# Optimization experiments

Measured on AMD Instinct MI355X. Metric: run time of the kernel, lower is better.

The kernel has to match this reference:

```python
import jax, jax.numpy as jnp
import numpy as np

B, S, H, DH, D, FD, FU = 4, 256, 12, 64, 768, 2048, 2048


def setup_inputs() -> dict:
    key = jax.random.key(0)
    ks = jax.random.split(key, 12)
    s = 0.02  # typical init scale for weights
    return {
        "resid_pre": jax.random.normal(ks[0], (B, S, D), jnp.float32),
        "ln_scale": jax.random.uniform(ks[1], (B, S, 1), jnp.float32, 0.5, 2.0),
        "probs": jax.nn.softmax(jax.random.normal(ks[2], (B, H, S, S), jnp.float32), axis=-1),
        "W_O": jax.random.normal(ks[3], (H, DH, D), jnp.float32) * s,
        "W_V": jax.random.normal(ks[4], (H, D, DH), jnp.float32) * s,
        "enc_W": jax.random.normal(ks[5], (FD, D), jnp.float32) * s,
        "enc_b": jax.random.normal(ks[6], (FD,), jnp.float32) * s,
        "b_dec": jax.random.normal(ks[7], (D,), jnp.float32) * s,
        "up_dec_W": jax.random.normal(ks[8], (D, FU), jnp.float32) * s,
        "up_b_dec": jax.random.normal(ks[9], (D,), jnp.float32) * s,
        "pruned_features": jax.random.normal(ks[10], (B, S, FU), jnp.float32),
        "connection_mask": jax.random.randint(ks[11], (FD, FU), 0, 2, jnp.int32),
    }


def reference(resid_pre, ln_scale, probs, W_O, W_V, enc_W, enc_b, b_dec,
              up_dec_W, up_b_dec, pruned_features, connection_mask):
    # W_OV: [h, d_model(in), d_model(out)]
    W_OV = jnp.einsum('hko,hmk->hmo', W_O, W_V)
    mask = connection_mask.astype(resid_pre.dtype)

    # --- initial contributions ---
    act_ln = resid_pre / ln_scale                                  # [b,s,d]
    pre_moving = jnp.einsum('bsi,hio,fo->bshf', act_ln, W_OV, enc_W)  # [b,s,h,f_down]
    approx = jnp.einsum('bhqk,bkhf->bqf', probs, pre_moving)       # [b,q,f_down]

    # --- pruned contributions (one upstream AE) ---
    virtual = jnp.einsum('fo,hio,iu->hfu', enc_W, W_OV, up_dec_W) * mask[None]
    up_ln = pruned_features / ln_scale                             # [b,k,f_up]
    post_ov = jnp.einsum('bku,hfu->bhkf', up_ln, virtual)          # [b,h,k,f_down]
    approx = approx + jnp.einsum('bhqk,bhkf->bqf', probs, post_ov)

    # --- bias terms ---
    approx = approx + enc_b[None, None] - (enc_W @ b_dec)[None, None]
    ub_ln = up_b_dec[None, None] / ln_scale                        # [b,s,d]
    ub_post = jnp.einsum('hmd,bsm->bsd', W_OV, ub_ln)              # attn path through OV
    approx = approx + jnp.einsum('fd,bsd->bsf', enc_W, ub_post)
    return approx
```

## Files before the change

### kernel.cpp

```cpp
#include <hip/hip_runtime.h>
#include <hip/hip_bf16.h>
#include <stdint.h>

typedef __bf16 bf16;
typedef __bf16 bf16x8 __attribute__((ext_vector_type(8)));
typedef __bf16 bf16x4 __attribute__((ext_vector_type(4)));
typedef float f32x4 __attribute__((ext_vector_type(4)));

#define AS1 __attribute__((address_space(1)))
#define AS3 __attribute__((address_space(3)))


__device__ __forceinline__ void gld16(const bf16* g, bf16* l) {
  __builtin_amdgcn_global_load_lds((AS1 void*)g, (AS3 void*)l, 16, 0, 0);
}

__global__ void k_sentinel(float* __restrict__ out) {
  int i = blockIdx.x * 256 + threadIdx.x;
  if (i < 2097152) out[i] = 1048576.0f;
}

__global__ void k_prep(const float* __restrict__ lns, float* __restrict__ invln,
                       const float* __restrict__ enc_W, bf16* __restrict__ encWb,
                       const float* __restrict__ probs, bf16* __restrict__ probsT,
                       const int* __restrict__ cmask, bf16* __restrict__ maskb,
                       const float* __restrict__ W_O, bf16* __restrict__ WOb,
                       const float* __restrict__ resid, bf16* __restrict__ Xb,
                       bf16* __restrict__ BgTail, long ldTail) {
  const int bid = blockIdx.x, t = threadIdx.x;
  if (bid < 1) {
    for (int k = 0; k < 4; k++) { int j = t + k * 256; invln[j] = 1.0f / lns[j]; }
  } else if (bid < 1537) {
    long idx = ((long)(bid - 1) * 256 + t) * 4;
    float4 v = *(const float4*)(enc_W + idx);
    bf16x4 o; o[0]=(bf16)v.x; o[1]=(bf16)v.y; o[2]=(bf16)v.z; o[3]=(bf16)v.w;
    *(bf16x4*)(encWb + idx) = o;
  } else if (bid < 4609) {
    long idx = ((long)(bid - 1537) * 256 + t) * 4;
    int s = (int)(idx & 255), q = (int)((idx >> 8) & 255);
    int hb = (int)(idx >> 16), h = hb % 12, b = hb / 12;
    float4 v = *(const float4*)(probs + idx);
    bf16x4 o; o[0]=(bf16)v.x; o[1]=(bf16)v.y; o[2]=(bf16)v.z; o[3]=(bf16)v.w;
    *(bf16x4*)(probsT + (long)b * 786432 + (long)q * 3072 + h * 256 + s) = o;
  } else if (bid < 8705) {
    long idx = ((long)(bid - 4609) * 256 + t) * 4;
    int4 v = *(const int4*)(cmask + idx);
    bf16x4 o; o[0]=(bf16)(float)v.x; o[1]=(bf16)(float)v.y;
    o[2]=(bf16)(float)v.z; o[3]=(bf16)(float)v.w;
    *(bf16x4*)(maskb + idx) = o;
  } else if (bid < 9857) {
    long idx = ((long)(bid - 8705) * 256 + t) * 4;
    int o = (int)(idx % 768), r = (int)((idx / 768) & 127), h = (int)(idx / (768 * 128));
    bf16x4 ov;
    if (r < 64) {
      float4 v = *(const float4*)(W_O + (long)(h * 64 + r) * 768 + o);
      ov[0]=(bf16)v.x; ov[1]=(bf16)v.y; ov[2]=(bf16)v.z; ov[3]=(bf16)v.w;
    } else { ov[0]=ov[1]=ov[2]=ov[3]=(bf16)0.0f; }
    *(bf16x4*)(WOb + idx) = ov;
  } else if (bid < 10625) {
    long idx = ((long)(bid - 9857) * 256 + t) * 4;
    float il = 1.0f / lns[idx / 768];
    float4 v = *(const float4*)(resid + idx);
    bf16x4 o; o[0]=(bf16)(v.x*il); o[1]=(bf16)(v.y*il);
    o[2]=(bf16)(v.z*il); o[3]=(bf16)(v.w*il);
    *(bf16x4*)(Xb + idx) = o;
  } else {
    long idx = ((long)(bid - 10625) * 256 + t) * 4;
    int f = (int)(idx / 768), d = (int)(idx % 768);
    float4 v = *(const float4*)(enc_W + idx);
    bf16x4 o; o[0]=(bf16)v.x; o[1]=(bf16)v.y; o[2]=(bf16)v.z; o[3]=(bf16)v.w;
    *(bf16x4*)(BgTail + (long)f * ldTail + d) = o;
  }
}

__global__ void k_prepT(const float* __restrict__ wv, bf16* __restrict__ WVt,
                        const float* __restrict__ wo, bf16* __restrict__ W_Ot,
                        const float* __restrict__ updW, bf16* __restrict__ updWt,
                        const float* __restrict__ pr, const float* __restrict__ lns,
                        bf16* __restrict__ Ut) {
  __shared__ float tile[32][33];
  const int bid = blockIdx.x;
  int lane = threadIdx.x & 31, rg = threadIdx.x >> 5;
  if (bid < 1152) {
    int r0 = bid;
    int x = r0 % 4, y = (r0 / 4) % 24, h = r0 / 96;
    int k0 = x * 32, i0 = y * 32;
    if (k0 < 64) {
      for (int r = rg; r < 32; r += 8)
        tile[r][lane] = wv[((long)(h * 768 + i0 + r)) * 64 + k0 + lane];
      __syncthreads();
      for (int r = rg; r < 32; r += 8)
        WVt[((long)h * 128 + k0 + r) * 768 + i0 + lane] = (bf16)tile[lane][r];
    } else {
      for (int r = rg; r < 32; r += 8)
        WVt[((long)h * 128 + k0 + r) * 768 + i0 + lane] = (bf16)0.0f;
    }
  } else if (bid < 1728) {
    int r0 = bid - 1152;
    int x = r0 % 2, y = (r0 / 2) % 24, h = r0 / 48;
    int k0 = x * 32, o0 = y * 32;
    for (int r = rg; r < 32; r += 8)
      tile[r][lane] = wo[((long)(h * 64 + k0 + r)) * 768 + o0 + lane];
    __syncthreads();
    for (int r = rg; r < 32; r += 8)
      W_Ot[((long)(h * 768 + o0 + r)) * 64 + k0 + lane] = (bf16)tile[lane][r];
  } else if (bid < 3264) {
    int r0 = bid - 1728;
    int u0 = (r0 % 64) * 32, i0 = (r0 / 64) * 32;
    for (int r = rg; r < 32; r += 8)
      tile[r][lane] = updW[((long)(i0 + r)) * 2048 + u0 + lane];
    __syncthreads();
    for (int r = rg; r < 32; r += 8)
      updWt[((long)(u0 + r)) * 768 + i0 + lane] = (bf16)tile[lane][r];
  } else {
    int r0 = bid - 3264;
    int u0 = (r0 % 64) * 32, s0 = ((r0 / 64) % 8) * 32, b = r0 / 512;
    for (int r = rg; r < 32; r += 8) {
      int s = s0 + r;
      tile[r][lane] = pr[((long)(b * 256 + s)) * 2048 + u0 + lane] *
                      (1.0f / lns[b * 256 + s]);
    }
    __syncthreads();
    for (int r = rg; r < 32; r += 8)
      Ut[((long)b * 2048 + u0 + r) * 256 + s0 + lane] = (bf16)tile[lane][r];
  }
}

__global__ void k_sred(const float* __restrict__ Sp, bf16* __restrict__ dst, long ldd) {
  int i = blockIdx.x * 256 + threadIdx.x;
  if (i < 196608) {
    long idx = (long)i * 4;
    int m = (int)(idx / 768), o = (int)(idx % 768);
    float4 v = *(const float4*)(Sp + idx);
    float4 a = *(const float4*)(Sp + 786432 + idx);
    float4 b = *(const float4*)(Sp + 2 * 786432 + idx);
    float4 c = *(const float4*)(Sp + 3 * 786432 + idx);
    v.x += a.x + b.x + c.x; v.y += a.y + b.y + c.y;
    v.z += a.z + b.z + c.z; v.w += a.w + b.w + c.w;
    bf16x4 ov;
    ov[0] = (bf16)v.x; ov[1] = (bf16)v.y; ov[2] = (bf16)v.z; ov[3] = (bf16)v.w;
    *(bf16x4*)(dst + (long)m * ldd + o) = ov;
  }
}


__device__ __forceinline__ float blk_reduce(float s) {
  __shared__ float red[256];
  red[threadIdx.x] = s; __syncthreads();
  for (int o = 128; o > 0; o >>= 1) {
    if ((int)threadIdx.x < o) red[threadIdx.x] += red[threadIdx.x + o];
    __syncthreads();
  }
  float r = red[0]; __syncthreads();
  return r;
}

__global__ void k_bias_t(const float* __restrict__ W_V, const float* __restrict__ up_b,
                         float* __restrict__ t_hk) {
  int j = blockIdx.x, h = j >> 6, k = j & 63;
  float s = 0.f;
  for (int m = threadIdx.x; m < 768; m += 256)
    s += W_V[((long)(h * 768 + m)) * 64 + k] * up_b[m];
  float r = blk_reduce(s);
  if (threadIdx.x == 0) t_hk[j] = r;
}

__global__ void k_bias_w(const float* __restrict__ W_O, const float* __restrict__ t_hk,
                         float* __restrict__ w) {
  int d = blockIdx.x;
  float s = 0.f;
  for (int j = threadIdx.x; j < 768; j += 256)
    s += W_O[(long)j * 768 + d] * t_hk[j];
  float r = blk_reduce(s);
  if (threadIdx.x == 0) w[d] = r;
}

__global__ void k_bias_c(const float* __restrict__ enc_W, const float* __restrict__ enc_b,
                         const float* __restrict__ b_dec, const float* __restrict__ w,
                         float* __restrict__ c0, float* __restrict__ c1) {
  int f = blockIdx.x;
  float s0 = 0.f, s1 = 0.f;
  for (int d = threadIdx.x; d < 768; d += 256) {
    float e = enc_W[(long)f * 768 + d];
    s0 += e * b_dec[d];
    s1 += e * w[d];
  }
  float r0 = blk_reduce(s0);
  float r1 = blk_reduce(s1);
  if (threadIdx.x == 0) { c0[f] = enc_b[f] - r0; c1[f] = r1; }
}

__global__ __launch_bounds__(256)
void gemm_bt(const bf16* __restrict__ A, const bf16* __restrict__ B, void* __restrict__ Cv,
             int M, int N, int K,
             long lda, long ldb, long ldc,
             int batchH,
             long sa_b, long sa_h, long sb_b, long sb_h, long sc_b, long sc_h,
             int mode, int kChunk,
             const bf16* __restrict__ mask, long mask_ld)
{
  __shared__ __align__(16) bf16 SMEM[16384];
  bf16* Asm = SMEM;
  bf16* Bsm = SMEM + 8192;

  const int t = threadIdx.x;

  const int nbx = gridDim.x, nby = gridDim.y;
  const int nxy = nbx * nby;
  int orig = blockIdx.x + nbx * blockIdx.y;
  int qq = nxy >> 3, rr = nxy & 7;
  int xcd = orig & 7, lid = orig >> 3;
  int swz = (xcd < rr) ? (xcd * (qq + 1) + lid)
                       : (rr * (qq + 1) + (xcd - rr) * qq + lid);
  const int m0 = (swz % nby) * 128;
  const int n0 = (swz / nby) * 128;

  long aoff, boff, coff;
  int k0, k1;
  if (mode == 4) {
    int z = blockIdx.z;
    int bb = z / batchH, kc = z - bb * batchH;
    aoff = (long)bb * sa_b;
    boff = (long)bb * sb_b;
    coff = (long)bb * sc_b + (long)kc * sc_h;
    k0 = kc * kChunk; k1 = k0 + kChunk; if (k1 > K) k1 = K;
  } else if (mode >= 2) {
    int z = blockIdx.z;
    aoff = 0; boff = 0;
    coff = (long)z * (long)M * ldc;
    k0 = z * kChunk; k1 = k0 + kChunk; if (k1 > K) k1 = K;
  } else {
    int z = blockIdx.z;
    int bb = z / batchH, hh = z - bb * batchH;
    aoff = (long)bb * sa_b + (long)hh * sa_h;
    boff = (long)bb * sb_b + (long)hh * sb_h;
    coff = (long)bb * sc_b + (long)hh * sc_h;
    k0 = 0; k1 = K;
  }

  const bf16* Ab = A + aoff + (long)m0 * lda;
  const bf16* Bb = B + boff + (long)n0 * ldb;

  const int r0 = t >> 3;
  const int g8 = t & 7;

  const int L = t & 63, w = t >> 6;
  const int wm = (w & 1) * 64, wn = (w >> 1) * 64;
  const int r16 = L & 15, q = L >> 4;

  f32x4 acc[4][4];
#pragma unroll
  for (int i = 0; i < 4; i++)
#pragma unroll
    for (int j = 0; j < 4; j++) acc[i][j] = (f32x4){0.f, 0.f, 0.f, 0.f};

  for (int kt = k0; kt < k1; kt += 64) {
#pragma unroll
    for (int j = 0; j < 4; j++) {
      int row = j * 32 + r0;
      int sc = ((g8 ^ (row & 7)) << 3);
      gld16(Ab + (long)row * lda + (kt + sc), &Asm[j * 2048 + t * 8]);
      gld16(Bb + (long)row * ldb + (kt + sc), &Bsm[j * 2048 + t * 8]);
    }
    __syncthreads();

#pragma unroll
    for (int h2 = 0; h2 < 2; h2++) {
      bf16x8 af[4], bfr[4];
#pragma unroll
      for (int i = 0; i < 4; i++) {
        int ra = wm + i * 16 + r16;
        af[i]  = *(const bf16x8*)&Asm[ra * 64 + ((((h2 << 2) + q) ^ (ra & 7)) << 3)];
        int rb = wn + i * 16 + r16;
        bfr[i] = *(const bf16x8*)&Bsm[rb * 64 + ((((h2 << 2) + q) ^ (rb & 7)) << 3)];
      }
#pragma unroll
      for (int mi = 0; mi < 4; mi++)
#pragma unroll
        for (int ni = 0; ni < 4; ni++)
          acc[mi][ni] = __builtin_amdgcn_mfma_f32_16x16x32_bf16(af[mi], bfr[ni], acc[mi][ni], 0, 0, 0);
    }
    __syncthreads();
  }

  if (mode >= 2) {
    float* C = (float*)Cv;
#pragma unroll
    for (int mi = 0; mi < 4; mi++)
#pragma unroll
      for (int ni = 0; ni < 4; ni++)
#pragma unroll
        for (int r = 0; r < 4; r++) {
          int gm = m0 + wm + mi * 16 + q * 4 + r;
          int gn = n0 + wn + ni * 16 + r16;
          long idx = coff + (long)gm * ldc + gn;
          float v = acc[mi][ni][r];
          if (mode == 3) v += C[idx];
          C[idx] = v;
        }
  } else {
    bf16* C = (bf16*)Cv;
    bf16* lbuf = SMEM;
    const int lrbase = (wm >> 6) * 32 + q * 4;
    const int lr_r = t >> 2;
    const int colg = (t & 3) * 32;
#pragma unroll
    for (int hh = 0; hh < 2; hh++) {
#pragma unroll
      for (int m2 = 0; m2 < 2; m2++) {
        int mi = hh * 2 + m2;
#pragma unroll
        for (int ni = 0; ni < 4; ni++) {
          int col = wn + ni * 16 + r16;
#pragma unroll
          for (int r = 0; r < 4; r++)
            lbuf[(lrbase + m2 * 16 + r) * 136 + col] = (bf16)acc[mi][ni][r];
        }
      }
      __syncthreads();
      int gm = m0 + (lr_r >> 5) * 64 + hh * 32 + (lr_r & 31);
#pragma unroll
      for (int s = 0; s < 4; s++) {
        bf16x8 v = *(const bf16x8*)&lbuf[lr_r * 136 + colg + 8 * s];
        int gn = n0 + colg + 8 * s;
        if (mode == 1) {
          bf16x8 mv = *(const bf16x8*)&mask[(long)gm * mask_ld + gn];
#pragma unroll
          for (int j = 0; j < 8; j++) v[j] = (bf16)((float)v[j] * (float)mv[j]);
        }
        *(bf16x8*)&C[coff + (long)gm * ldc + gn] = v;
      }
      __syncthreads();
    }
  }
}

__global__ __launch_bounds__(512, 2)
void gemm_fp2(const bf16* __restrict__ A, const bf16* __restrict__ B,
              float* __restrict__ C,
              int M, int N, int K, long lda, long ldb, long ldc,
              int mode, int kChunk)
{
  __shared__ __align__(16) bf16 SM[2][2][16384];

  const int t = threadIdx.x;

  const int nz = gridDim.z;
  int fid = blockIdx.x + gridDim.x * (blockIdx.y + gridDim.y * blockIdx.z);
  const int z  = fid % nz;
  const int t2 = fid / nz;
  const int m0 = (t2 >> 3) * 256;
  const int n0 = (t2 & 7) * 256;

  const long coff = (long)z * (long)M * ldc;
  int k0 = z * kChunk, k1 = k0 + kChunk; if (k1 > K) k1 = K;
  const int NT = (k1 > k0) ? (k1 - k0) >> 6 : 0;

  const bf16* Ab = A + (long)m0 * lda + k0;
  const bf16* Bb = B + (long)n0 * ldb + k0;

  const int sr = t >> 3;
  const int g8 = t & 7;

  const int L = t & 63, w = t >> 6;
  const int wm = (w & 1) * 128;
  const int wn = (w >> 1) * 64;
  const int r16 = L & 15, q = L >> 4;

  f32x4 acc[8][4];
#pragma unroll
  for (int i = 0; i < 8; i++)
#pragma unroll
    for (int j = 0; j < 4; j++) acc[i][j] = (f32x4){0.f, 0.f, 0.f, 0.f};

  auto stage = [&](int tt, int buf) {
    const bf16* Ap = Ab + (long)tt * 64;
    const bf16* Bp = Bb + (long)tt * 64;
#pragma unroll
    for (int j = 0; j < 4; j++) {
      int row = j * 64 + sr;
      int sc = ((g8 ^ (row & 7)) << 3);
      gld16(Ap + (long)row * lda + sc, &SM[buf][0][j * 4096 + t * 8]);
    }
#pragma unroll
    for (int j = 0; j < 4; j++) {
      int row = j * 64 + sr;
      int sc = ((g8 ^ (row & 7)) << 3);
      gld16(Bp + (long)row * ldb + sc, &SM[buf][1][j * 4096 + t * 8]);
    }
  };

  if (NT >= 1) stage(0, 0);

  for (int tt = 0; tt < NT; tt++) {
    if (tt + 1 < NT) {
      stage(tt + 1, (tt + 1) & 1);
      asm volatile("s_waitcnt vmcnt(8)" ::: "memory");
    } else {
      asm volatile("s_waitcnt vmcnt(0)" ::: "memory");
    }
    __builtin_amdgcn_s_barrier();

    const bf16* As = &SM[tt & 1][0][0];
    const bf16* Bs = &SM[tt & 1][1][0];
#pragma unroll
    for (int h2 = 0; h2 < 2; h2++) {
      bf16x8 af[8], bfr[4];
#pragma unroll
      for (int i = 0; i < 8; i++) {
        int ra = wm + i * 16 + r16;
        af[i]  = *(const bf16x8*)&As[ra * 64 + ((((h2 << 2) + q) ^ (ra & 7)) << 3)];
      }
#pragma unroll
      for (int i = 0; i < 4; i++) {
        int rb = wn + i * 16 + r16;
        bfr[i] = *(const bf16x8*)&Bs[rb * 64 + ((((h2 << 2) + q) ^ (rb & 7)) << 3)];
      }
#pragma unroll
      for (int mi = 0; mi < 8; mi++)
#pragma unroll
        for (int ni = 0; ni < 4; ni++)
          acc[mi][ni] = __builtin_amdgcn_mfma_f32_16x16x32_bf16(af[mi], bfr[ni], acc[mi][ni], 0, 0, 0);
    }
    __builtin_amdgcn_s_barrier();
  }

#pragma unroll
  for (int mi = 0; mi < 8; mi++)
#pragma unroll
    for (int ni = 0; ni < 4; ni++)
#pragma unroll
      for (int r = 0; r < 4; r++) {
        int gm = m0 + wm + mi * 16 + q * 4 + r;
        int gn = n0 + wn + ni * 16 + r16;
        long idx = coff + (long)gm * ldc + gn;
        float v = acc[mi][ni][r];
        if (mode == 3) v += C[idx];
        C[idx] = v;
      }
}

__global__ void k_out(const float* __restrict__ Cp, const float* __restrict__ c0,
                      const float* __restrict__ c1, const float* __restrict__ invln,
                      float* __restrict__ out, int nsplit) {
  int i4 = blockIdx.x * 256 + threadIdx.x;
  long i = (long)i4 * 4;
  int n = (int)(i & 2047), m = (int)(i >> 11);
  float4 v = *(const float4*)(Cp + i);
  for (int z = 1; z < nsplit; z++) {
    float4 u = *(const float4*)(Cp + i + (long)z * 2097152);
    v.x += u.x; v.y += u.y; v.z += u.z; v.w += u.w;
  }
  float il = invln[m];
  float4 a = *(const float4*)(c0 + n);
  float4 b = *(const float4*)(c1 + n);
  v.x += a.x + b.x * il;
  v.y += a.y + b.y * il;
  v.z += a.z + b.z * il;
  v.w += a.w + b.w * il;
  *(float4*)(out + i) = v;
}


extern "C" void kernel_launch(void* const* d_in, const int* in_sizes, int n_in,
                              void* d_out, int out_size, void* d_ws, size_t ws_size,
                              hipStream_t stream) {
  (void)out_size;
  float* out = (float*)d_out;

  int iresid = -1, iln = -1, iprobs = -1, iencb = -1, ipruned = -1, imask = -1;
  int iwo = -1, iwv = -1, iencw = -1, iupdw = -1, ibdec = -1, iupb = -1;
  for (int i = 0; i < n_in; i++) {
    switch (in_sizes[i]) {
      case 786432:  iresid  = i; break;
      case 1024:    iln     = i; break;
      case 3145728: iprobs  = i; break;
      case 2048:    iencb   = i; break;
      case 2097152: ipruned = i; break;
      case 4194304: imask   = i; break;
      case 589824:  if (iwo   < 0) iwo   = i; else iwv   = i; break;
      case 1572864: if (iencw < 0) iencw = i; else iupdw = i; break;
      case 768:     if (ibdec < 0) ibdec = i; else iupb  = i; break;
      default: break;
    }
  }
  bool ok = n_in == 12 && iresid >= 0 && iln >= 0 && iprobs >= 0 && iencb >= 0 &&
            ipruned >= 0 && imask >= 0 && iwo >= 0 && iwv >= 0 && iencw >= 0 &&
            iupdw >= 0 && ibdec >= 0 && iupb >= 0;
  if (!ok) { k_sentinel<<<8192, 256, 0, stream>>>(out); return; }

  const float* resid = (const float*)d_in[iresid];
  const float* lns   = (const float*)d_in[iln];
  const float* probs = (const float*)d_in[iprobs];
  const float* W_O   = (const float*)d_in[iwo];
  const float* W_V   = (const float*)d_in[iwv];
  const float* enc_W = (const float*)d_in[iencw];
  const float* enc_b = (const float*)d_in[iencb];
  const float* b_dec = (const float*)d_in[ibdec];
  const float* updW  = (const float*)d_in[iupdw];
  const float* up_b  = (const float*)d_in[iupb];
  const float* pruned= (const float*)d_in[ipruned];
  const int*   cmask = (const int*)d_in[imask];

  auto pad = [](size_t b) -> size_t { return (b + 255) & ~(size_t)255; };
  const size_t prepB = pad(2359296) + pad(2359296) + pad(3145728) + pad(1572864) +
                       pad(3145728) + pad(1179648) + pad(3145728) + pad(18874368) +
                       pad(12582912);
  const size_t persB = pad(6291456) + pad(4194304) + pad(6291456) + pad(6291456) +
                       pad(8388608) + pad(4096) + pad(3072) + pad(3072) +
                       pad(8192) + pad(8192);
  auto needB = [&](int g, int ns) -> size_t {
    size_t cp = (size_t)ns * 8388608;
    size_t ov = prepB > cp ? prepB : cp;
    long KA = (long)g * 2048 + 768;
    size_t ab = pad((size_t)1024 * KA * 2) + pad((size_t)2048 * KA * 2);
    return ov + persB + ab + (2ull << 20);
  };
  const int cgs[14] = {12, 12, 12, 6, 6, 4, 3, 2, 2, 1, 1, 1, 1, 1};
  const int cns[14] = { 8,  4, 2, 8, 4, 4, 4, 4, 2, 8, 4, 2, 2, 1};
  int gs = 0, nsplit = 0;
  for (int ci = 0; ci < 14; ci++) {
    if (needB(cgs[ci], cns[ci]) <= ws_size) { gs = cgs[ci]; nsplit = cns[ci]; break; }
  }
  if (gs == 0) { gs = 1; nsplit = 1; }

  const long KA = (long)gs * 2048 + 768;

  char* p = (char*)d_ws;
  auto alloc = [&](size_t bytes) -> char* {
    char* r = p; p += (bytes + 255) & ~(size_t)255; return r;
  };
  char* overlayBase = p;
  bf16*  WOb    = (bf16*)alloc(12ull * 128 * 768 * 2);
  bf16*  WVt    = (bf16*)alloc(12ull * 128 * 768 * 2);
  bf16*  updWt  = (bf16*)alloc(2048ull * 768 * 2);
  bf16*  Xb     = (bf16*)alloc(1024ull * 768 * 2);
  bf16*  encWb  = (bf16*)alloc(2048ull * 768 * 2);
  bf16*  W_Ot   = (bf16*)alloc(12ull * 768 * 64 * 2);
  bf16*  T1     = (bf16*)alloc(12ull * 1024 * 128 * 2);
  bf16*  T3     = (bf16*)alloc(4ull * 768 * 3072 * 2);
  float* Sp     = (float*)alloc(4ull * 1024 * 768 * 4);
  {
    size_t used = (size_t)(p - overlayBase);
    size_t cp = (size_t)nsplit * 8388608;
    p = overlayBase + (used > cp ? used : cp);
  }
  float* Cpart  = (float*)overlayBase;
  bf16*  G_t    = (bf16*)alloc(12ull * 2048 * 128 * 2);
  bf16*  Ut     = (bf16*)alloc(4ull * 2048 * 256 * 2);
  bf16*  E1     = (bf16*)alloc(12ull * 2048 * 128 * 2);
  bf16*  probsT = (bf16*)alloc(4ull * 256 * 3072 * 2);
  bf16*  maskb  = (bf16*)alloc(2048ull * 2048 * 2);
  float* invln  = (float*)alloc(1024 * 4);
  float* t_hk   = (float*)alloc(768 * 4);
  float* wv     = (float*)alloc(768 * 4);
  float* c0     = (float*)alloc(2048 * 4);
  float* c1     = (float*)alloc(2048 * 4);
  bf16*  A_g    = (bf16*)alloc((size_t)1024 * KA * 2);
  bf16*  B_g    = (bf16*)alloc((size_t)2048 * KA * 2);

  k_prep<<<12161, 256, 0, stream>>>(lns, invln, enc_W, encWb, probs, probsT,
                                    cmask, maskb, W_O, WOb, resid, Xb,
                                    B_g + (long)gs * 2048, KA);
  k_prepT<<<5312, 256, 0, stream>>>(W_V, WVt, W_O, W_Ot, updW, updWt,
                                    pruned, lns, Ut);
  k_bias_t<<<768, 256, 0, stream>>>(W_V, up_b, t_hk);
  k_bias_w<<<768, 256, 0, stream>>>(W_O, t_hk, wv);
  k_bias_c<<<2048, 256, 0, stream>>>(enc_W, enc_b, b_dec, wv, c0, c1);

  gemm_bt<<<dim3(1, 16, 24), 256, 0, stream>>>(
      encWb, WOb, E1, 2048, 128, 768,
      768, 768, 128, 12,
      (long)(updWt - encWb), 0,
      (long)(WVt - WOb), (long)128 * 768,
      (long)(G_t - E1), (long)2048 * 128,
      0, 0, nullptr, 0);

  gemm_bt<<<dim3(1, 8, 12), 256, 0, stream>>>(
      Xb, WVt, T1, 1024, 128, 768,
      768, 768, 128, 12,
      0, 0, 0, (long)128 * 768, 0, (long)1024 * 128,
      0, 0, nullptr, 0);

  gemm_bt<<<dim3(2, 6, 48), 256, 0, stream>>>(
      W_Ot, T1, T3, 768, 256, 64,
      64, 128, 3072, 12,
      0, (long)768 * 64, (long)256 * 128, (long)1024 * 128, 2359296, 256,
      0, 0, nullptr, 0);

  gemm_bt<<<dim3(6, 2, 16), 256, 0, stream>>>(
      probsT, T3, Sp, 256, 768, 3072,
      3072, 3072, 768, 4,
      786432, 0, 2359296, 0, 196608, 786432,
      4, 768, nullptr, 0);

  k_sred<<<768, 256, 0, stream>>>(Sp, A_g + (long)gs * 2048, KA);

  for (int g = 0; g < 12 / gs; g++) {
    gemm_bt<<<dim3(16, 16, gs), 256, 0, stream>>>(
        E1 + (long)g * gs * 2048 * 128, G_t + (long)g * gs * 2048 * 128, B_g,
        2048, 2048, 64,
        128, 128, KA, gs,
        0, (long)2048 * 128, 0, (long)2048 * 128, 0, 2048,
        1, 0, maskb, 2048);

    gemm_bt<<<dim3(16, 2, 4 * gs), 256, 0, stream>>>(
        probsT + (long)g * gs * 256, Ut, A_g,
        256, 2048, 256,
        3072, 256, KA, gs,
        786432, 256, (long)2048 * 256, 0, 256 * KA, 2048,
        0, 0, nullptr, 0);

    int Kthis = (g == 0) ? (int)KA : gs * 2048;
    int kc = ((Kthis / nsplit + 63) / 64) * 64;
    gemm_fp2<<<dim3(8, 4, nsplit), 512, 0, stream>>>(
        A_g, B_g, Cpart,
        1024, 2048, Kthis,
        KA, KA, 2048,
        (g == 0) ? 2 : 3, kc);
  }

  k_out<<<2048, 256, 0, stream>>>(Cpart, c0, c1, invln, out, nsplit);
}
```

Measured before the change: 406.7 us.

## Fuse bias, reduction and batched GEMM launches into fewer kernels

The three bias kernels are folded into extra blocks of the prep, transpose and split-reduce kernels. The E1/G_t GEMM and the X·W_V GEMM become one batched launch: buffers are laid out contiguously and the third batch clamps its B operand and exits early beyond its smaller M. The per-group loop is replaced by a single pass over all heads. The goal is to cut launch count and serial tail gaps, at the cost of assuming the full group size fits in memory.

```diff
diff --git a/kernel.cpp b/kernel.cpp
--- a/kernel.cpp
+++ b/kernel.cpp
@@ -26,7 +26,10 @@
                        const int* __restrict__ cmask, bf16* __restrict__ maskb,
                        const float* __restrict__ W_O, bf16* __restrict__ WOb,
                        const float* __restrict__ resid, bf16* __restrict__ Xb,
-                       bf16* __restrict__ BgTail, long ldTail) {
+                       bf16* __restrict__ BgTail, long ldTail,
+                       const float* __restrict__ W_V, const float* __restrict__ up_b,
+                       float* __restrict__ t_hk) {
+  __shared__ float red[256];
   const int bid = blockIdx.x, t = threadIdx.x;
   if (bid < 1) {
     for (int k = 0; k < 4; k++) { int j = t + k * 256; invln[j] = 1.0f / lns[j]; }
@@ -64,12 +67,21 @@
     bf16x4 o; o[0]=(bf16)(v.x*il); o[1]=(bf16)(v.y*il);
     o[2]=(bf16)(v.z*il); o[3]=(bf16)(v.w*il);
     *(bf16x4*)(Xb + idx) = o;
-  } else {
+  } else if (bid < 12161) {
     long idx = ((long)(bid - 10625) * 256 + t) * 4;
     int f = (int)(idx / 768), d = (int)(idx % 768);
     float4 v = *(const float4*)(enc_W + idx);
     bf16x4 o; o[0]=(bf16)v.x; o[1]=(bf16)v.y; o[2]=(bf16)v.z; o[3]=(bf16)v.w;
     *(bf16x4*)(BgTail + (long)f * ldTail + d) = o;
+  } else {
+    int h = bid - 12161;
+    int k = t & 63, qd = t >> 6;
+    float s = 0.f;
+    for (int m = qd; m < 768; m += 4)
+      s += W_V[((long)(h * 768 + m)) * 64 + k] * up_b[m];
+    red[t] = s; __syncthreads();
+    if (qd == 0)
+      t_hk[h * 64 + k] = red[k] + red[64 + k] + red[128 + k] + red[192 + k];
   }
 }
 
@@ -77,7 +89,8 @@
                         const float* __restrict__ wo, bf16* __restrict__ W_Ot,
                         const float* __restrict__ updW, bf16* __restrict__ updWt,
                         const float* __restrict__ pr, const float* __restrict__ lns,
-                        bf16* __restrict__ Ut) {
+                        bf16* __restrict__ Ut,
+                        const float* __restrict__ t_hk, float* __restrict__ wvec) {
   __shared__ float tile[32][33];
   const int bid = blockIdx.x;
   int lane = threadIdx.x & 31, rg = threadIdx.x >> 5;
@@ -112,7 +125,7 @@
     __syncthreads();
     for (int r = rg; r < 32; r += 8)
       updWt[((long)(u0 + r)) * 768 + i0 + lane] = (bf16)tile[lane][r];
-  } else {
+  } else if (bid < 5312) {
     int r0 = bid - 3264;
     int u0 = (r0 % 64) * 32, s0 = ((r0 / 64) % 8) * 32, b = r0 / 512;
     for (int r = rg; r < 32; r += 8) {
@@ -123,12 +136,29 @@
     __syncthreads();
     for (int r = rg; r < 32; r += 8)
       Ut[((long)b * 2048 + u0 + r) * 256 + s0 + lane] = (bf16)tile[lane][r];
-  }
-}
-
-__global__ void k_sred(const float* __restrict__ Sp, bf16* __restrict__ dst, long ldd) {
-  int i = blockIdx.x * 256 + threadIdx.x;
-  if (i < 196608) {
+  } else {
+    int d = bid - 5312;
+    float* red = &tile[0][0];
+    float s = 0.f;
+    for (int j = threadIdx.x; j < 768; j += 256)
+      s += wo[(long)j * 768 + d] * t_hk[j];
+    red[threadIdx.x] = s; __syncthreads();
+    for (int o = 128; o > 0; o >>= 1) {
+      if ((int)threadIdx.x < o) red[threadIdx.x] += red[threadIdx.x + o];
+      __syncthreads();
+    }
+    if (threadIdx.x == 0) wvec[d] = red[0];
+  }
+}
+
+__global__ void k_misc(const float* __restrict__ Sp, bf16* __restrict__ dst, long ldd,
+                       const float* __restrict__ enc_W, const float* __restrict__ enc_b,
+                       const float* __restrict__ b_dec, const float* __restrict__ w,
+                       float* __restrict__ c0, float* __restrict__ c1) {
+  __shared__ float red[512];
+  const int bid = blockIdx.x, t = threadIdx.x;
+  if (bid < 768) {
+    int i = bid * 256 + t;
     long idx = (long)i * 4;
     int m = (int)(idx / 768), o = (int)(idx % 768);
     float4 v = *(const float4*)(Sp + idx);
@@ -140,54 +170,21 @@
     bf16x4 ov;
     ov[0] = (bf16)v.x; ov[1] = (bf16)v.y; ov[2] = (bf16)v.z; ov[3] = (bf16)v.w;
     *(bf16x4*)(dst + (long)m * ldd + o) = ov;
-  }
-}
-
-
-__device__ __forceinline__ float blk_reduce(float s) {
-  __shared__ float red[256];
-  red[threadIdx.x] = s; __syncthreads();
-  for (int o = 128; o > 0; o >>= 1) {
-    if ((int)threadIdx.x < o) red[threadIdx.x] += red[threadIdx.x + o];
-    __syncthreads();
-  }
-  float r = red[0]; __syncthreads();
-  return r;
-}
-
-__global__ void k_bias_t(const float* __restrict__ W_V, const float* __restrict__ up_b,
-                         float* __restrict__ t_hk) {
-  int j = blockIdx.x, h = j >> 6, k = j & 63;
-  float s = 0.f;
-  for (int m = threadIdx.x; m < 768; m += 256)
-    s += W_V[((long)(h * 768 + m)) * 64 + k] * up_b[m];
-  float r = blk_reduce(s);
-  if (threadIdx.x == 0) t_hk[j] = r;
-}
-
-__global__ void k_bias_w(const float* __restrict__ W_O, const float* __restrict__ t_hk,
-                         float* __restrict__ w) {
-  int d = blockIdx.x;
-  float s = 0.f;
-  for (int j = threadIdx.x; j < 768; j += 256)
-    s += W_O[(long)j * 768 + d] * t_hk[j];
-  float r = blk_reduce(s);
-  if (threadIdx.x == 0) w[d] = r;
-}
-
-__global__ void k_bias_c(const float* __restrict__ enc_W, const float* __restrict__ enc_b,
-                         const float* __restrict__ b_dec, const float* __restrict__ w,
-                         float* __restrict__ c0, float* __restrict__ c1) {
-  int f = blockIdx.x;
-  float s0 = 0.f, s1 = 0.f;
-  for (int d = threadIdx.x; d < 768; d += 256) {
-    float e = enc_W[(long)f * 768 + d];
-    s0 += e * b_dec[d];
-    s1 += e * w[d];
-  }
-  float r0 = blk_reduce(s0);
-  float r1 = blk_reduce(s1);
-  if (threadIdx.x == 0) { c0[f] = enc_b[f] - r0; c1[f] = r1; }
+  } else {
+    int f = bid - 768;
+    float s0 = 0.f, s1 = 0.f;
+    for (int d = t; d < 768; d += 256) {
+      float e = enc_W[(long)f * 768 + d];
+      s0 += e * b_dec[d];
+      s1 += e * w[d];
+    }
+    red[t] = s0; red[256 + t] = s1; __syncthreads();
+    for (int o = 128; o > 0; o >>= 1) {
+      if (t < o) { red[t] += red[t + o]; red[256 + t] += red[256 + t + o]; }
+      __syncthreads();
+    }
+    if (t == 0) { c0[f] = enc_b[f] - red[0]; c1[f] = red[256]; }
+  }
 }
 
 __global__ __launch_bounds__(256)
@@ -197,7 +194,8 @@
              int batchH,
              long sa_b, long sa_h, long sb_b, long sb_h, long sc_b, long sc_h,
              int mode, int kChunk,
-             const bf16* __restrict__ mask, long mask_ld)
+             const bf16* __restrict__ mask, long mask_ld,
+             int bbBmax, int bbM2)
 {
   __shared__ __align__(16) bf16 SMEM[16384];
   bf16* Asm = SMEM;
@@ -232,8 +230,10 @@
   } else {
     int z = blockIdx.z;
     int bb = z / batchH, hh = z - bb * batchH;
+    if (bbM2 && bb >= 2 && m0 >= bbM2) return;
+    int bbB = bb < bbBmax ? bb : bbBmax;
     aoff = (long)bb * sa_b + (long)hh * sa_h;
-    boff = (long)bb * sb_b + (long)hh * sb_h;
+    boff = (long)bbB * sb_b + (long)hh * sb_h;
     coff = (long)bb * sc_b + (long)hh * sc_h;
     k0 = 0; k1 = K;
   }
@@ -502,18 +502,23 @@
   const float* pruned= (const float*)d_in[ipruned];
   const int*   cmask = (const int*)d_in[imask];
 
-  auto pad = [](size_t b) -> size_t { return (b + 255) & ~(size_t)255; };
-  const size_t prepB = pad(2359296) + pad(2359296) + pad(3145728) + pad(1572864) +
-                       pad(3145728) + pad(1179648) + pad(3145728) + pad(18874368) +
-                       pad(12582912);
-  const size_t persB = pad(6291456) + pad(4194304) + pad(6291456) + pad(6291456) +
-                       pad(8388608) + pad(4096) + pad(3072) + pad(3072) +
-                       pad(8192) + pad(8192);
+  const size_t prepB =
+      2359296ull + 2359296ull
+    + 3145728ull * 3
+    + 1179648ull
+    + 6291456ull * 3
+    + 4194304ull
+    + 6291456ull
+    + 8388608ull
+    + 18874368ull
+    + 12582912ull
+    + 3072ull + 3072ull + 512;
+  const size_t persB = 4096 + 8192 + 8192 + 768;
   auto needB = [&](int g, int ns) -> size_t {
     size_t cp = (size_t)ns * 8388608;
     size_t ov = prepB > cp ? prepB : cp;
     long KA = (long)g * 2048 + 768;
-    size_t ab = pad((size_t)1024 * KA * 2) + pad((size_t)2048 * KA * 2);
+    size_t ab = (size_t)1024 * KA * 2 + 256 + (size_t)2048 * KA * 2 + 256;
     return ov + persB + ab + (2ull << 20);
   };
   const int cgs[14] = {12, 12, 12, 6, 6, 4, 3, 2, 2, 1, 1, 1, 1, 1};
@@ -531,93 +536,88 @@
     char* r = p; p += (bytes + 255) & ~(size_t)255; return r;
   };
   char* overlayBase = p;
-  bf16*  WOb    = (bf16*)alloc(12ull * 128 * 768 * 2);
-  bf16*  WVt    = (bf16*)alloc(12ull * 128 * 768 * 2);
-  bf16*  updWt  = (bf16*)alloc(2048ull * 768 * 2);
-  bf16*  Xb     = (bf16*)alloc(1024ull * 768 * 2);
-  bf16*  encWb  = (bf16*)alloc(2048ull * 768 * 2);
-  bf16*  W_Ot   = (bf16*)alloc(12ull * 768 * 64 * 2);
-  bf16*  T1     = (bf16*)alloc(12ull * 1024 * 128 * 2);
-  bf16*  T3     = (bf16*)alloc(4ull * 768 * 3072 * 2);
-  float* Sp     = (float*)alloc(4ull * 1024 * 768 * 4);
+  bf16*  WOb    = (bf16*)alloc(2359296);
+  bf16*  WVt    = (bf16*)alloc(2359296);
+  bf16*  encWb  = (bf16*)alloc(3145728);
+  bf16*  updWt  = (bf16*)alloc(3145728);
+  bf16*  Xb     = (bf16*)alloc(3145728);
+  bf16*  W_Ot   = (bf16*)alloc(1179648);
+  bf16*  E1     = (bf16*)alloc(6291456);
+  bf16*  G_t    = (bf16*)alloc(6291456);
+  bf16*  T1     = (bf16*)alloc(6291456);
+  bf16*  Ut     = (bf16*)alloc(4194304);
+  bf16*  probsT = (bf16*)alloc(6291456);
+  bf16*  maskb  = (bf16*)alloc(8388608);
+  bf16*  T3     = (bf16*)alloc(18874368);
+  float* Sp     = (float*)alloc(12582912);
+  float* t_hk   = (float*)alloc(3072);
+  float* wvec   = (float*)alloc(3072);
   {
     size_t used = (size_t)(p - overlayBase);
     size_t cp = (size_t)nsplit * 8388608;
     p = overlayBase + (used > cp ? used : cp);
   }
   float* Cpart  = (float*)overlayBase;
-  bf16*  G_t    = (bf16*)alloc(12ull * 2048 * 128 * 2);
-  bf16*  Ut     = (bf16*)alloc(4ull * 2048 * 256 * 2);
-  bf16*  E1     = (bf16*)alloc(12ull * 2048 * 128 * 2);
-  bf16*  probsT = (bf16*)alloc(4ull * 256 * 3072 * 2);
-  bf16*  maskb  = (bf16*)alloc(2048ull * 2048 * 2);
   float* invln  = (float*)alloc(1024 * 4);
-  float* t_hk   = (float*)alloc(768 * 4);
-  float* wv     = (float*)alloc(768 * 4);
   float* c0     = (float*)alloc(2048 * 4);
   float* c1     = (float*)alloc(2048 * 4);
   bf16*  A_g    = (bf16*)alloc((size_t)1024 * KA * 2);
   bf16*  B_g    = (bf16*)alloc((size_t)2048 * KA * 2);
 
-  k_prep<<<12161, 256, 0, stream>>>(lns, invln, enc_W, encWb, probs, probsT,
+  const int BIG = 1 << 30;
+
+  k_prep<<<12173, 256, 0, stream>>>(lns, invln, enc_W, encWb, probs, probsT,
                                     cmask, maskb, W_O, WOb, resid, Xb,
-                                    B_g + (long)gs * 2048, KA);
-  k_prepT<<<5312, 256, 0, stream>>>(W_V, WVt, W_O, W_Ot, updW, updWt,
-                                    pruned, lns, Ut);
-  k_bias_t<<<768, 256, 0, stream>>>(W_V, up_b, t_hk);
-  k_bias_w<<<768, 256, 0, stream>>>(W_O, t_hk, wv);
-  k_bias_c<<<2048, 256, 0, stream>>>(enc_W, enc_b, b_dec, wv, c0, c1);
-
-  gemm_bt<<<dim3(1, 16, 24), 256, 0, stream>>>(
+                                    B_g + (long)gs * 2048, KA,
+                                    W_V, up_b, t_hk);
+  k_prepT<<<6080, 256, 0, stream>>>(W_V, WVt, W_O, W_Ot, updW, updWt,
+                                    pruned, lns, Ut, t_hk, wvec);
+
+  gemm_bt<<<dim3(1, 16, 36), 256, 0, stream>>>(
       encWb, WOb, E1, 2048, 128, 768,
       768, 768, 128, 12,
-      (long)(updWt - encWb), 0,
+      1572864, 0,
       (long)(WVt - WOb), (long)128 * 768,
-      (long)(G_t - E1), (long)2048 * 128,
-      0, 0, nullptr, 0);
-
-  gemm_bt<<<dim3(1, 8, 12), 256, 0, stream>>>(
-      Xb, WVt, T1, 1024, 128, 768,
-      768, 768, 128, 12,
-      0, 0, 0, (long)128 * 768, 0, (long)1024 * 128,
-      0, 0, nullptr, 0);
+      3145728, (long)2048 * 128,
+      0, 0, nullptr, 0, 1, 1024);
 
   gemm_bt<<<dim3(2, 6, 48), 256, 0, stream>>>(
       W_Ot, T1, T3, 768, 256, 64,
       64, 128, 3072, 12,
-      0, (long)768 * 64, (long)256 * 128, (long)1024 * 128, 2359296, 256,
-      0, 0, nullptr, 0);
+      0, (long)768 * 64, 32768, 262144, 2359296, 256,
+      0, 0, nullptr, 0, BIG, 0);
 
   gemm_bt<<<dim3(6, 2, 16), 256, 0, stream>>>(
       probsT, T3, Sp, 256, 768, 3072,
       3072, 3072, 768, 4,
       786432, 0, 2359296, 0, 196608, 786432,
-      4, 768, nullptr, 0);
-
-  k_sred<<<768, 256, 0, stream>>>(Sp, A_g + (long)gs * 2048, KA);
-
-  for (int g = 0; g < 12 / gs; g++) {
-    gemm_bt<<<dim3(16, 16, gs), 256, 0, stream>>>(
-        E1 + (long)g * gs * 2048 * 128, G_t + (long)g * gs * 2048 * 128, B_g,
-        2048, 2048, 64,
-        128, 128, KA, gs,
-        0, (long)2048 * 128, 0, (long)2048 * 128, 0, 2048,
-        1, 0, maskb, 2048);
-
-    gemm_bt<<<dim3(16, 2, 4 * gs), 256, 0, stream>>>(
-        probsT + (long)g * gs * 256, Ut, A_g,
-        256, 2048, 256,
-        3072, 256, KA, gs,
-        786432, 256, (long)2048 * 256, 0, 256 * KA, 2048,
-        0, 0, nullptr, 0);
-
-    int Kthis = (g == 0) ? (int)KA : gs * 2048;
+      4, 768, nullptr, 0, BIG, 0);
+
+  k_misc<<<2816, 256, 0, stream>>>(Sp, A_g + (long)gs * 2048, KA,
+                                   enc_W, enc_b, b_dec, wvec, c0, c1);
+
+  gemm_bt<<<dim3(16, 16, gs), 256, 0, stream>>>(
+      E1, G_t, B_g,
+      2048, 2048, 64,
+      128, 128, KA, gs,
+      0, (long)2048 * 128, 0, (long)2048 * 128, 0, 2048,
+      1, 0, maskb, 2048, BIG, 0);
+
+  gemm_bt<<<dim3(16, 2, 4 * gs), 256, 0, stream>>>(
+      probsT, Ut, A_g,
+      256, 2048, 256,
+      3072, 256, KA, gs,
+      786432, 256, (long)2048 * 256, 0, 256 * KA, 2048,
+      0, 0, nullptr, 0, BIG, 0);
+
+  {
+    int Kthis = (int)KA;
     int kc = ((Kthis / nsplit + 63) / 64) * 64;
     gemm_fp2<<<dim3(8, 4, nsplit), 512, 0, stream>>>(
         A_g, B_g, Cpart,
         1024, 2048, Kthis,
         KA, KA, 2048,
-        (g == 0) ? 2 : 3, kc);
+        2, kc);
   }
 
   k_out<<<2048, 256, 0, stream>>>(Cpart, c0, c1, invln, out, nsplit);
```

After: 469.5 us. 1.15x slower.
